# Optimization experiments

Measured on AMD Instinct MI355X. Metric: run time of the kernel, lower is better.

Reference implementation:

```python
import jax, jax.numpy as jnp
import numpy as np

D = 64
H = 4
HD = D // H
N_MOL, E_MOL = 2048, 32768
N_PROT, E_PROT = 8192, 262144
LN_EPS = 1e-5


def _lin_params(key, d_in, d_out):
    k1, k2 = jax.random.split(key)
    lim = 1.0 / np.sqrt(d_in)
    w = jax.random.uniform(k1, (d_in, d_out), minval=-lim, maxval=lim, dtype=jnp.float32)
    b = jax.random.uniform(k2, (d_out,), minval=-lim, maxval=lim, dtype=jnp.float32)
    return w, b


def setup_inputs() -> dict:
    key = jax.random.key(0)
    ks = jax.random.split(key, 20)
    inp = {
        'x_mol': jax.random.normal(ks[0], (N_MOL, D), dtype=jnp.float32),
        'edge_index_mol': jax.random.randint(ks[1], (2, E_MOL), 0, N_MOL),
        'edge_attr_mol': jax.random.normal(ks[2], (E_MOL, D), dtype=jnp.float32),
        'x_prot': jax.random.normal(ks[3], (N_PROT, D), dtype=jnp.float32),
        'edge_index_prot': jax.random.randint(ks[4], (2, E_PROT), 0, N_PROT),
        'edge_attr_prot': jax.random.normal(ks[5], (E_PROT, D), dtype=jnp.float32),
    }
    # GINE MLPs: Linear -> ReLU -> Linear
    inp['mol_w1'], inp['mol_b1'] = _lin_params(ks[6], D, D)
    inp['mol_w2'], inp['mol_b2'] = _lin_params(ks[7], D, D)
    inp['prot_w1'], inp['prot_b1'] = _lin_params(ks[8], D, D)
    inp['prot_w2'], inp['prot_b2'] = _lin_params(ks[9], D, D)
    # cross-attn mol->prot (query=mol, key/value=prot)
    inp['mp_wq'], inp['mp_bq'] = _lin_params(ks[10], D, D)
    inp['mp_wk'], inp['mp_bk'] = _lin_params(ks[11], D, D)
    inp['mp_wv'], inp['mp_bv'] = _lin_params(ks[12], D, D)
    # cross-attn prot->mol (query=prot, key/value=mol)
    inp['pm_wq'], inp['pm_bq'] = _lin_params(ks[13], D, D)
    inp['pm_wk'], inp['pm_bk'] = _lin_params(ks[14], D, D)
    inp['pm_wv'], inp['pm_bv'] = _lin_params(ks[15], D, D)
    # layer norms
    inp['ln_mol_g'] = jnp.ones((D,), jnp.float32)
    inp['ln_mol_b'] = jnp.zeros((D,), jnp.float32)
    inp['ln_prot_g'] = jnp.ones((D,), jnp.float32)
    inp['ln_prot_b'] = jnp.zeros((D,), jnp.float32)
    return inp


def _gine_conv(x, edge_index, edge_attr, w1, b1, w2, b2, n_nodes):
    # message: relu(x_j + edge_attr); aggregate: mean at target; update: MLP((1+eps)*x + aggr), eps=0
    src, dst = edge_index[0], edge_index[1]
    msg = jax.nn.relu(x[src] + edge_attr)                       # [E, D]
    ssum = jax.ops.segment_sum(msg, dst, num_segments=n_nodes)  # [N, D]
    cnt = jax.ops.segment_sum(jnp.ones((msg.shape[0],), msg.dtype), dst, num_segments=n_nodes)
    aggr = ssum / jnp.maximum(cnt, 1.0)[:, None]
    h = x + aggr
    h = jax.nn.relu(h @ w1 + b1) @ w2 + b2
    return h


def _cross_attn(q_nodes, k_nodes, wq, bq, wk, bk, wv, bv):
    Nq, Nk = q_nodes.shape[0], k_nodes.shape[0]
    Q = (q_nodes @ wq + bq).reshape(Nq, H, HD)
    K = (k_nodes @ wk + bk).reshape(Nk, H, HD)
    V = (k_nodes @ wv + bv).reshape(Nk, H, HD)
    scores = jnp.einsum('qhd,khd->hqk', Q, K) / np.sqrt(HD).astype(np.float32)
    attn = jax.nn.softmax(scores, axis=-1)                      # [H, Nq, Nk]
    out = jnp.einsum('hqk,khd->qhd', attn, V).reshape(Nq, D)
    return out


def _layer_norm(x, g, b):
    mu = jnp.mean(x, axis=-1, keepdims=True)
    var = jnp.mean(jnp.square(x - mu), axis=-1, keepdims=True)
    return (x - mu) * jax.lax.rsqrt(var + LN_EPS) * g + b


def reference(x_mol, edge_index_mol, edge_attr_mol, x_prot, edge_index_prot, edge_attr_prot,
              mol_w1, mol_b1, mol_w2, mol_b2, prot_w1, prot_b1, prot_w2, prot_b2,
              mp_wq, mp_bq, mp_wk, mp_bk, mp_wv, mp_bv,
              pm_wq, pm_bq, pm_wk, pm_bk, pm_wv, pm_bv,
              ln_mol_g, ln_mol_b, ln_prot_g, ln_prot_b):
    h_mol = jax.nn.relu(_gine_conv(x_mol, edge_index_mol, edge_attr_mol,
                                   mol_w1, mol_b1, mol_w2, mol_b2, x_mol.shape[0]))
    h_prot = jax.nn.relu(_gine_conv(x_prot, edge_index_prot, edge_attr_prot,
                                    prot_w1, prot_b1, prot_w2, prot_b2, x_prot.shape[0]))
    h_mol_attn = _cross_attn(h_mol, h_prot, mp_wq, mp_bq, mp_wk, mp_bk, mp_wv, mp_bv)
    h_prot_attn = _cross_attn(h_prot, h_mol, pm_wq, pm_bq, pm_wk, pm_bk, pm_wv, pm_bv)
    out_mol = _layer_norm(h_mol + h_mol_attn, ln_mol_g, ln_mol_b)
    out_prot = _layer_norm(h_prot + h_prot_attn, ln_prot_g, ln_prot_b)
    return out_mol, out_prot
```

## Files before the change

kernel.cpp:

```cpp
#include <hip/hip_runtime.h>

#define NM 2048
#define EM 32768
#define NP 8192
#define EP 262144

typedef __attribute__((ext_vector_type(8))) short short8;
typedef __attribute__((ext_vector_type(4))) short short4v;
typedef __attribute__((ext_vector_type(4))) float f32x4;
typedef __attribute__((ext_vector_type(16))) float f32x16;

#define LOG2E 1.44269504088896340736f

__device__ __forceinline__ float e2(float x) { return __builtin_amdgcn_exp2f(x); }
__device__ __forceinline__ unsigned int pk_bf16_tr(float a, float b) {
    return __builtin_amdgcn_perm(__float_as_uint(a), __float_as_uint(b), 0x03020706u);
}
__device__ __forceinline__ unsigned short cvt_bf16(float f) {
    unsigned int u = __float_as_uint(f);
    u = (u + 0x7fff + ((u >> 16) & 1)) >> 16;
    return (unsigned short)u;
}

__global__ __launch_bounds__(256) void hist_kernel(
    const int* __restrict__ ei_m, const int* __restrict__ ei_p,
    int* __restrict__ cnt_m, int* __restrict__ cnt_p)
{
    int idx = blockIdx.x * 256 + threadIdx.x;
    if (idx < EM) atomicAdd(&cnt_m[ei_m[EM + idx]], 1);
    int j = idx - EM;
    if (j >= 0 && j < EP) atomicAdd(&cnt_p[ei_p[EP + j]], 1);
}

__global__ __launch_bounds__(256) void scan_kernel(
    const int* __restrict__ cnt_m, const int* __restrict__ cnt_p,
    int* __restrict__ start_m, int* __restrict__ start_p,
    int* __restrict__ cur_m, int* __restrict__ cur_p)
{
    const int* cnt; int* start; int* cur; int n;
    if (blockIdx.x == 0) { cnt = cnt_m; start = start_m; cur = cur_m; n = NM; }
    else                 { cnt = cnt_p; start = start_p; cur = cur_p; n = NP; }
    int per = n >> 8;
    int tid = threadIdx.x;
    int base = tid * per;
    int s = 0;
    for (int i = 0; i < per; i++) s += cnt[base + i];
    __shared__ int wsum[4];
    int lane = tid & 63, w = tid >> 6;
    int v = s;
    #pragma unroll
    for (int off = 1; off < 64; off <<= 1) {
        int u = __shfl_up(v, off, 64);
        if (lane >= off) v += u;
    }
    if (lane == 63) wsum[w] = v;
    __syncthreads();
    int wo = 0;
    for (int i = 0; i < w; i++) wo += wsum[i];
    int run = wo + v - s;
    for (int i = 0; i < per; i++) {
        start[base + i] = run; cur[base + i] = run;
        run += cnt[base + i];
    }
    if (tid == 255) start[n] = run;
}

__global__ __launch_bounds__(256) void scatter_kernel(
    const int* __restrict__ ei_m, const int* __restrict__ ei_p,
    int* __restrict__ cur_m, int* __restrict__ cur_p,
    int* __restrict__ pidx_m, int* __restrict__ pidx_p)
{
    int idx = blockIdx.x * 256 + threadIdx.x;
    if (idx < EM) {
        int d = ei_m[EM + idx];
        int pos = atomicAdd(&cur_m[d], 1);
        pidx_m[pos] = (idx << 11) | ei_m[idx];
    }
    int j = idx - EM;
    if (j >= 0 && j < EP) {
        int d = ei_p[EP + j];
        int pos = atomicAdd(&cur_p[d], 1);
        pidx_p[pos] = (j << 13) | ei_p[j];
    }
}

__global__ __launch_bounds__(256) void node_aggr_kernel(
    const float* __restrict__ x_m, const float* __restrict__ ea_m,
    const int* __restrict__ start_m, const int* __restrict__ pidx_m,
    const float* __restrict__ x_p, const float* __restrict__ ea_p,
    const int* __restrict__ start_p, const int* __restrict__ pidx_p,
    unsigned short* __restrict__ h0b_m, unsigned short* __restrict__ h0b_p)
{
    int wave = threadIdx.x >> 6, lane = threadIdx.x & 63;
    int nid = blockIdx.x * 4 + wave;
    const float *x, *ea; const int *start, *pidx; unsigned short* h0b; int n, sh, msk;
    if (nid < NM) { x = x_m; ea = ea_m; start = start_m; pidx = pidx_m; h0b = h0b_m; n = nid; sh = 11; msk = 2047; }
    else          { x = x_p; ea = ea_p; start = start_p; pidx = pidx_p; h0b = h0b_p; n = nid - NM; sh = 13; msk = 8191; }
    int b  = __builtin_amdgcn_readfirstlane(start[n]);
    int e  = __builtin_amdgcn_readfirstlane(start[n + 1]);
    int deg = e - b;
    const int* pp = pidx + b;
    float acc = 0.f;
    int j = 0;
    for (; j + 8 <= deg; j += 8) {
        int v0 = __builtin_amdgcn_readfirstlane(pp[j]);
        int v1 = __builtin_amdgcn_readfirstlane(pp[j + 1]);
        int v2 = __builtin_amdgcn_readfirstlane(pp[j + 2]);
        int v3 = __builtin_amdgcn_readfirstlane(pp[j + 3]);
        int v4 = __builtin_amdgcn_readfirstlane(pp[j + 4]);
        int v5 = __builtin_amdgcn_readfirstlane(pp[j + 5]);
        int v6 = __builtin_amdgcn_readfirstlane(pp[j + 6]);
        int v7 = __builtin_amdgcn_readfirstlane(pp[j + 7]);
        float a0 = ea[(size_t)(((unsigned)v0) >> sh) * 64 + lane];
        float a1 = ea[(size_t)(((unsigned)v1) >> sh) * 64 + lane];
        float a2 = ea[(size_t)(((unsigned)v2) >> sh) * 64 + lane];
        float a3 = ea[(size_t)(((unsigned)v3) >> sh) * 64 + lane];
        float a4 = ea[(size_t)(((unsigned)v4) >> sh) * 64 + lane];
        float a5 = ea[(size_t)(((unsigned)v5) >> sh) * 64 + lane];
        float a6 = ea[(size_t)(((unsigned)v6) >> sh) * 64 + lane];
        float a7 = ea[(size_t)(((unsigned)v7) >> sh) * 64 + lane];
        float y0 = x[(size_t)(v0 & msk) * 64 + lane];
        float y1 = x[(size_t)(v1 & msk) * 64 + lane];
        float y2 = x[(size_t)(v2 & msk) * 64 + lane];
        float y3 = x[(size_t)(v3 & msk) * 64 + lane];
        float y4 = x[(size_t)(v4 & msk) * 64 + lane];
        float y5 = x[(size_t)(v5 & msk) * 64 + lane];
        float y6 = x[(size_t)(v6 & msk) * 64 + lane];
        float y7 = x[(size_t)(v7 & msk) * 64 + lane];
        acc += fmaxf(y0 + a0, 0.f); acc += fmaxf(y1 + a1, 0.f);
        acc += fmaxf(y2 + a2, 0.f); acc += fmaxf(y3 + a3, 0.f);
        acc += fmaxf(y4 + a4, 0.f); acc += fmaxf(y5 + a5, 0.f);
        acc += fmaxf(y6 + a6, 0.f); acc += fmaxf(y7 + a7, 0.f);
    }
    for (; j < deg; ++j) {
        int v0 = __builtin_amdgcn_readfirstlane(pp[j]);
        acc += fmaxf(x[(size_t)(v0 & msk) * 64 + lane] + ea[(size_t)(((unsigned)v0) >> sh) * 64 + lane], 0.f);
    }
    float aggr = acc / fmaxf((float)deg, 1.f);
    h0b[(size_t)n * 64 + lane] = cvt_bf16(x[(size_t)n * 64 + lane] + aggr);
}

__global__ __launch_bounds__(256) void prep_w_kernel(
    const float* __restrict__ w0, const float* __restrict__ w1, const float* __restrict__ w2,
    const float* __restrict__ w3, const float* __restrict__ w4, const float* __restrict__ w5,
    const float* __restrict__ w6, const float* __restrict__ w7, const float* __restrict__ w8,
    const float* __restrict__ w9, unsigned short* __restrict__ wt)
{
    int b = blockIdx.x;
    int t = b >> 4;
    int e = (b & 15) * 256 + threadIdx.x;
    const float* src;
    switch (t) {
        case 0: src = w0; break; case 1: src = w1; break; case 2: src = w2; break;
        case 3: src = w3; break; case 4: src = w4; break; case 5: src = w5; break;
        case 6: src = w6; break; case 7: src = w7; break; case 8: src = w8; break;
        default: src = w9; break;
    }
    int n = e >> 6, k = e & 63;
    wt[t * 4096 + e] = cvt_bf16(src[k * 64 + n]);
}

__global__ __launch_bounds__(256) void mlp_qkv_kernel(
    const unsigned short* __restrict__ h0b_m, const unsigned short* __restrict__ h0b_p,
    const unsigned short* __restrict__ wt,
    const float* __restrict__ b1m_, const float* __restrict__ b2m_,
    const float* __restrict__ bqm_, const float* __restrict__ bkm_, const float* __restrict__ bvm_,
    const float* __restrict__ b1p_, const float* __restrict__ b2p_,
    const float* __restrict__ bqp_, const float* __restrict__ bkp_, const float* __restrict__ bvp_,
    float* __restrict__ hm, float* __restrict__ hp,
    unsigned short* __restrict__ Qm, unsigned short* __restrict__ Km, unsigned short* __restrict__ Vtm,
    unsigned short* __restrict__ Qp, unsigned short* __restrict__ Kp, unsigned short* __restrict__ Vtp,
    int* __restrict__ norms)
{
    __shared__ unsigned short tile[4][2][16][72];
    int t = threadIdx.x, wave = t >> 6, lane = t & 63;
    int col = lane & 15, quad = lane >> 4;
    int blk = blockIdx.x;
    const unsigned short* h0b; const float *b1, *b2, *bq, *bk, *bv;
    float* hout; unsigned short *Q, *K, *Vt; int N, row0, wofs, nb;
    if (blk < NM / 64) {
        h0b = h0b_m; b1 = b1m_; b2 = b2m_; bq = bqm_; bk = bkm_; bv = bvm_;
        hout = hm; Q = Qm; K = Km; Vt = Vtm; N = NM;
        row0 = blk * 64 + wave * 16; wofs = 0; nb = 0;
    } else {
        h0b = h0b_p; b1 = b1p_; b2 = b2p_; bq = bqp_; bk = bkp_; bv = bvp_;
        hout = hp; Q = Qp; K = Kp; Vt = Vtp; N = NP;
        row0 = (blk - NM / 64) * 64 + wave * 16; wofs = 5 * 4096; nb = 2;
    }
    const f32x4 zero4 = {0.f, 0.f, 0.f, 0.f};
    const unsigned short* wb = wt + wofs + (size_t)col * 64 + quad * 8;

    const unsigned short* ar = h0b + (size_t)(row0 + col) * 64 + quad * 8;
    short8 aL = *(const short8*)ar;
    short8 aH = *(const short8*)(ar + 32);

    #pragma unroll
    for (int nt = 0; nt < 4; ++nt) {
        short8 bL = *(const short8*)(wb + nt * 1024);
        short8 bH = *(const short8*)(wb + nt * 1024 + 32);
        f32x4 d = __builtin_amdgcn_mfma_f32_16x16x32_bf16(aL, bL, zero4, 0, 0, 0);
        d = __builtin_amdgcn_mfma_f32_16x16x32_bf16(aH, bH, d, 0, 0, 0);
        float bias = b1[nt * 16 + col];
        #pragma unroll
        for (int r = 0; r < 4; ++r)
            tile[wave][0][quad * 4 + r][nt * 16 + col] = cvt_bf16(fmaxf(d[r] + bias, 0.f));
    }
    short8 a1L = *(const short8*)&tile[wave][0][col][quad * 8];
    short8 a1H = *(const short8*)&tile[wave][0][col][32 + quad * 8];

    #pragma unroll
    for (int nt = 0; nt < 4; ++nt) {
        short8 bL = *(const short8*)(wb + 4096 + nt * 1024);
        short8 bH = *(const short8*)(wb + 4096 + nt * 1024 + 32);
        f32x4 d = __builtin_amdgcn_mfma_f32_16x16x32_bf16(a1L, bL, zero4, 0, 0, 0);
        d = __builtin_amdgcn_mfma_f32_16x16x32_bf16(a1H, bH, d, 0, 0, 0);
        float bias = b2[nt * 16 + col];
        #pragma unroll
        for (int r = 0; r < 4; ++r) {
            float v = fmaxf(d[r] + bias, 0.f);
            hout[(size_t)(row0 + quad * 4 + r) * 64 + nt * 16 + col] = v;
            tile[wave][1][quad * 4 + r][nt * 16 + col] = cvt_bf16(v);
        }
    }
    short8 a2L = *(const short8*)&tile[wave][1][col][quad * 8];
    short8 a2H = *(const short8*)&tile[wave][1][col][32 + quad * 8];

    float q2[4] = {0.f, 0.f, 0.f, 0.f};
    #pragma unroll
    for (int nt = 0; nt < 4; ++nt) {
        short8 bL = *(const short8*)(wb + 2 * 4096 + nt * 1024);
        short8 bH = *(const short8*)(wb + 2 * 4096 + nt * 1024 + 32);
        f32x4 d = __builtin_amdgcn_mfma_f32_16x16x32_bf16(a2L, bL, zero4, 0, 0, 0);
        d = __builtin_amdgcn_mfma_f32_16x16x32_bf16(a2H, bH, d, 0, 0, 0);
        float bias = bq[nt * 16 + col];
        #pragma unroll
        for (int r = 0; r < 4; ++r) {
            float qv = (d[r] + bias) * (0.25f * LOG2E);
            Q[(size_t)(row0 + quad * 4 + r) * 64 + nt * 16 + col] = cvt_bf16(qv);
            q2[r] += qv * qv;
        }
    }
    float qmx = 0.f;
    #pragma unroll
    for (int r = 0; r < 4; ++r) {
        float s = q2[r];
        s += __shfl_xor(s, 1, 64); s += __shfl_xor(s, 2, 64);
        s += __shfl_xor(s, 4, 64); s += __shfl_xor(s, 8, 64);
        qmx = fmaxf(qmx, s);
    }

    float k2[4] = {0.f, 0.f, 0.f, 0.f};
    #pragma unroll
    for (int nt = 0; nt < 4; ++nt) {
        short8 bL = *(const short8*)(wb + 3 * 4096 + nt * 1024);
        short8 bH = *(const short8*)(wb + 3 * 4096 + nt * 1024 + 32);
        f32x4 d = __builtin_amdgcn_mfma_f32_16x16x32_bf16(a2L, bL, zero4, 0, 0, 0);
        d = __builtin_amdgcn_mfma_f32_16x16x32_bf16(a2H, bH, d, 0, 0, 0);
        float bias = bk[nt * 16 + col];
        #pragma unroll
        for (int r = 0; r < 4; ++r) {
            float kv = d[r] + bias;
            K[(size_t)(row0 + quad * 4 + r) * 64 + nt * 16 + col] = cvt_bf16(kv);
            k2[r] += kv * kv;
        }
    }
    float kmx = 0.f;
    #pragma unroll
    for (int r = 0; r < 4; ++r) {
        float s = k2[r];
        s += __shfl_xor(s, 1, 64); s += __shfl_xor(s, 2, 64);
        s += __shfl_xor(s, 4, 64); s += __shfl_xor(s, 8, 64);
        kmx = fmaxf(kmx, s);
    }

    #pragma unroll
    for (int nt = 0; nt < 4; ++nt) {
        short8 bL = *(const short8*)(wb + 4 * 4096 + nt * 1024);
        short8 bH = *(const short8*)(wb + 4 * 4096 + nt * 1024 + 32);
        f32x4 d = __builtin_amdgcn_mfma_f32_16x16x32_bf16(a2L, bL, zero4, 0, 0, 0);
        d = __builtin_amdgcn_mfma_f32_16x16x32_bf16(a2H, bH, d, 0, 0, 0);
        float bias = bv[nt * 16 + col];
        short4v vv;
        vv.x = (short)cvt_bf16(d[0] + bias);
        vv.y = (short)cvt_bf16(d[1] + bias);
        vv.z = (short)cvt_bf16(d[2] + bias);
        vv.w = (short)cvt_bf16(d[3] + bias);
        *(short4v*)(Vt + (size_t)(nt * 16 + col) * N + row0 + quad * 4) = vv;
    }

    qmx = fmaxf(qmx, __shfl_xor(qmx, 16, 64)); qmx = fmaxf(qmx, __shfl_xor(qmx, 32, 64));
    kmx = fmaxf(kmx, __shfl_xor(kmx, 16, 64)); kmx = fmaxf(kmx, __shfl_xor(kmx, 32, 64));
    if (lane == 0) {
        atomicMax(&norms[nb],     __float_as_int(sqrtf(qmx)));
        atomicMax(&norms[nb + 1], __float_as_int(sqrtf(kmx)));
    }
}

__global__ __launch_bounds__(256) void attn_kernel(
    const unsigned short* __restrict__ Qm, const unsigned short* __restrict__ Km,
    const unsigned short* __restrict__ Vtm,
    const unsigned short* __restrict__ Qp, const unsigned short* __restrict__ Kp,
    const unsigned short* __restrict__ Vtp,
    const int* __restrict__ norms, float* __restrict__ partial)
{
    __shared__ unsigned int plds[4][2][2][16][20];
    int t = threadIdx.x;
    int wave = t >> 6;
    int lane = t & 63;
    int qrow = lane & 15;
    int quad = lane >> 4;
    int q5   = lane & 31;
    int half = lane >> 5;
    int qtl  = q5 >> 4;
    int dwb  = half * 2;
    int W = blockIdx.x * 4 + wave;

    const unsigned short *Q, *K, *Vt; int Nk; float m;
    int chunk, h, qt2, Tbase, T1off;
    if (W < 2048) {
        Q = Qm; K = Kp; Vt = Vtp; Nk = NP;
        m = __int_as_float(norms[0]) * __int_as_float(norms[3]);
        chunk = W & 7; h = (W >> 3) & 3; qt2 = W >> 5;
        Tbase = W + qt2 * 32; T1off = 32;
    } else {
        int W2 = W - 2048;
        Q = Qp; K = Km; Vt = Vtm; Nk = NM;
        m = __int_as_float(norms[2]) * __int_as_float(norms[1]);
        chunk = W2 & 1; h = (W2 >> 1) & 3; qt2 = W2 >> 3;
        Tbase = 4096 + W2 + qt2 * 8; T1off = 8;
    }

    short8 qf = *(const short8*)(Q + ((size_t)(qt2 * 32 + q5)) * 64 + h * 16 + half * 8);

    const f32x16 zero16 = {0.f,0.f,0.f,0.f,0.f,0.f,0.f,0.f,0.f,0.f,0.f,0.f,0.f,0.f,0.f,0.f};
    const f32x4 zero4 = {0.f, 0.f, 0.f, 0.f};
    int kbase = chunk * 1024;
    const unsigned short* krow = K + (size_t)(kbase + q5) * 64 + h * 16 + half * 8;
    const unsigned short* vrow = Vt + ((size_t)(h * 16 + qrow)) * Nk + kbase + quad * 8;

    float l = 0.0f;
    f32x4 accA = zero4, accB = zero4;

    short8 kf_0, kf_1, vf_0, vf_1;
    kf_0 = *(const short8*)(krow);
    kf_1 = *(const short8*)(krow + 32 * 64);
    vf_0 = *(const short8*)(vrow);
    vf_1 = *(const short8*)(vrow + 32);

    short8 vf_prev;

#define QK_PHASE(IT, SLOT, BUF)                                                             \
    {                                                                                       \
        short8 kf = kf_##SLOT; short8 vf = vf_##SLOT;                                       \
        if ((IT) < 30) {                                                                    \
            int off = ((IT) + 2) * 32;                                                      \
            kf_##SLOT = *(const short8*)(krow + (size_t)off * 64);                          \
            vf_##SLOT = *(const short8*)(vrow + off);                                       \
        }                                                                                   \
        f32x16 s = __builtin_amdgcn_mfma_f32_32x32x16_bf16(kf, qf, zero16, 0, 0, 0);        \
        float p0  = e2(s[0] - m),  p1  = e2(s[1] - m),  p2  = e2(s[2] - m),  p3  = e2(s[3] - m);  \
        float p4  = e2(s[4] - m),  p5  = e2(s[5] - m),  p6  = e2(s[6] - m),  p7  = e2(s[7] - m);  \
        float p8  = e2(s[8] - m),  p9  = e2(s[9] - m),  p10 = e2(s[10] - m), p11 = e2(s[11] - m); \
        float p12 = e2(s[12] - m), p13 = e2(s[13] - m), p14 = e2(s[14] - m), p15 = e2(s[15] - m); \
        l += (((p0 + p1) + (p2 + p3)) + ((p4 + p5) + (p6 + p7)))                            \
           + (((p8 + p9) + (p10 + p11)) + ((p12 + p13) + (p14 + p15)));                     \
        uint2 w0; w0.x = pk_bf16_tr(p0, p1);   w0.y = pk_bf16_tr(p2, p3);                   \
        uint2 w1; w1.x = pk_bf16_tr(p4, p5);   w1.y = pk_bf16_tr(p6, p7);                   \
        uint2 w2; w2.x = pk_bf16_tr(p8, p9);   w2.y = pk_bf16_tr(p10, p11);                 \
        uint2 w3; w3.x = pk_bf16_tr(p12, p13); w3.y = pk_bf16_tr(p14, p15);                 \
        *(uint2*)&plds[wave][qtl][BUF][qrow][dwb]      = w0;                                \
        *(uint2*)&plds[wave][qtl][BUF][qrow][dwb + 4]  = w1;                                \
        *(uint2*)&plds[wave][qtl][BUF][qrow][dwb + 8]  = w2;                                \
        *(uint2*)&plds[wave][qtl][BUF][qrow][dwb + 12] = w3;                                \
        vf_cur = vf;                                                                        \
    }

#define STEP(IT, SLOT, BUF, PREV)                                                           \
    {                                                                                       \
        short8 pfA = *(short8*)&plds[wave][0][PREV][qrow][quad * 4];                        \
        short8 pfB = *(short8*)&plds[wave][1][PREV][qrow][quad * 4];                        \
        short8 vf_cur;                                                                      \
        QK_PHASE(IT, SLOT, BUF)                                                             \
        accA = __builtin_amdgcn_mfma_f32_16x16x32_bf16(vf_prev, pfA, accA, 0, 0, 0);        \
        accB = __builtin_amdgcn_mfma_f32_16x16x32_bf16(vf_prev, pfB, accB, 0, 0, 0);        \
        vf_prev = vf_cur;                                                                   \
    }

    {
        short8 vf_cur;
        QK_PHASE(0, 0, 0)
        vf_prev = vf_cur;
    }
    for (int p = 0; p < 15; ++p) {
        STEP(2 * p + 1, 1, 1, 0)
        STEP(2 * p + 2, 0, 0, 1)
    }
    STEP(31, 1, 1, 0)
    {
        short8 pfA = *(short8*)&plds[wave][0][1][qrow][quad * 4];
        short8 pfB = *(short8*)&plds[wave][1][1][qrow][quad * 4];
        accA = __builtin_amdgcn_mfma_f32_16x16x32_bf16(vf_prev, pfA, accA, 0, 0, 0);
        accB = __builtin_amdgcn_mfma_f32_16x16x32_bf16(vf_prev, pfB, accB, 0, 0, 0);
    }
#undef STEP
#undef QK_PHASE

    float ltot = l + __shfl_xor(l, 32, 64);

    float* pb0 = partial + (size_t)Tbase * 288;
    *(f32x4*)&pb0[qrow * 16 + quad * 4] = accA;
    float* pb1 = partial + (size_t)(Tbase + T1off) * 288;
    *(f32x4*)&pb1[qrow * 16 + quad * 4] = accB;
    if (lane < 16)       pb0[272 + q5] = ltot;
    else if (lane < 32)  pb1[272 + (q5 - 16)] = ltot;
}

__global__ __launch_bounds__(256) void merge_ln_kernel(
    const float* __restrict__ partial,
    const float* __restrict__ h_m, const float* __restrict__ h_p,
    const float* __restrict__ gm, const float* __restrict__ bm,
    const float* __restrict__ gp, const float* __restrict__ bp_,
    float* __restrict__ out)
{
    int t = threadIdx.x;
    int grow = blockIdx.x * 4 + (t >> 6);
    int c = t & 63;
    const float *pbase, *hbuf, *g, *bb; float* o; int NC, row;
    if (grow < NM) { pbase = partial;               hbuf = h_m; g = gm; bb = bm;  o = out;             NC = 8; row = grow; }
    else           { pbase = partial + 4096 * 288;  hbuf = h_p; g = gp; bb = bp_; o = out + NM * 64;   NC = 2; row = grow - NM; }
    int hi = c >> 4, d = c & 15;
    int qt = row >> 4, ql = row & 15;
    const float* base = pbase + (size_t)(qt * 4 + hi) * NC * 288;
    float L = 0.0f, A = 0.0f;
    for (int cc = 0; cc < NC; ++cc) {
        L += base[cc * 288 + 272 + ql];
        A += base[cc * 288 + ql * 16 + d];
    }
    float v = hbuf[(size_t)row * 64 + c] + A / L;
    float s = v;
    #pragma unroll
    for (int o2 = 32; o2 >= 1; o2 >>= 1) s += __shfl_xor(s, o2, 64);
    float mu = s * (1.0f / 64.0f);
    float dv = v - mu;
    float sq = dv * dv;
    #pragma unroll
    for (int o2 = 32; o2 >= 1; o2 >>= 1) sq += __shfl_xor(sq, o2, 64);
    float var = sq * (1.0f / 64.0f);
    o[(size_t)row * 64 + c] = dv * rsqrtf(var + 1e-5f) * g[c] + bb[c];
}

extern "C" void kernel_launch(void* const* d_in, const int* in_sizes, int n_in,
                              void* d_out, int out_size, void* d_ws, size_t ws_size,
                              hipStream_t stream)
{
    const float* x_mol   = (const float*)d_in[0];
    const int*   ei_mol  = (const int*)  d_in[1];
    const float* ea_mol  = (const float*)d_in[2];
    const float* x_prot  = (const float*)d_in[3];
    const int*   ei_prot = (const int*)  d_in[4];
    const float* ea_prot = (const float*)d_in[5];
    const float* mol_w1  = (const float*)d_in[6];
    const float* mol_b1  = (const float*)d_in[7];
    const float* mol_w2  = (const float*)d_in[8];
    const float* mol_b2  = (const float*)d_in[9];
    const float* prot_w1 = (const float*)d_in[10];
    const float* prot_b1 = (const float*)d_in[11];
    const float* prot_w2 = (const float*)d_in[12];
    const float* prot_b2 = (const float*)d_in[13];
    const float* mp_wq = (const float*)d_in[14]; const float* mp_bq = (const float*)d_in[15];
    const float* mp_wk = (const float*)d_in[16]; const float* mp_bk = (const float*)d_in[17];
    const float* mp_wv = (const float*)d_in[18]; const float* mp_bv = (const float*)d_in[19];
    const float* pm_wq = (const float*)d_in[20]; const float* pm_bq = (const float*)d_in[21];
    const float* pm_wk = (const float*)d_in[22]; const float* pm_bk = (const float*)d_in[23];
    const float* pm_wv = (const float*)d_in[24]; const float* pm_bv = (const float*)d_in[25];
    const float* ln_mol_g  = (const float*)d_in[26];
    const float* ln_mol_b  = (const float*)d_in[27];
    const float* ln_prot_g = (const float*)d_in[28];
    const float* ln_prot_b = (const float*)d_in[29];

    float* ws = (float*)d_ws;
    float* h_mol   = ws;
    float* h_prot  = h_mol + 131072;
    float* partial = h_prot + 524288;
    unsigned short* h0b_mol  = (unsigned short*)partial;
    unsigned short* h0b_prot = h0b_mol + 131072;
    int* ip      = (int*)(partial + 2359296);
    int* cnt_m   = ip;
    int* cnt_p   = cnt_m + 2048;
    int* norms   = cnt_p + 8192;
    int* start_m = norms + 4;
    int* start_p = start_m + 2052;
    int* cur_m   = start_p + 8196;
    int* cur_p   = cur_m + 2048;
    int* pidx_m  = cur_p + 8192;
    int* pidx_p  = pidx_m + 32768;
    unsigned short* bf = (unsigned short*)(pidx_p + 262144);
    unsigned short* Qm  = bf;
    unsigned short* Km  = Qm + 131072;
    unsigned short* Vtm = Km + 131072;
    unsigned short* Qp  = Vtm + 131072;
    unsigned short* Kp  = Qp + 524288;
    unsigned short* Vtp = Kp + 524288;
    unsigned short* wt  = Vtp + 524288;

    hipMemsetAsync(cnt_m, 0, (size_t)(2048 + 8192 + 4) * sizeof(int), stream);

    prep_w_kernel<<<160, 256, 0, stream>>>(
        mol_w1, mol_w2, mp_wq, pm_wk, pm_wv,
        prot_w1, prot_w2, pm_wq, mp_wk, mp_wv, wt);

    const int EB = (EM + EP) / 256;
    hist_kernel<<<EB, 256, 0, stream>>>(ei_mol, ei_prot, cnt_m, cnt_p);
    scan_kernel<<<2, 256, 0, stream>>>(cnt_m, cnt_p, start_m, start_p, cur_m, cur_p);
    scatter_kernel<<<EB, 256, 0, stream>>>(ei_mol, ei_prot, cur_m, cur_p, pidx_m, pidx_p);
    node_aggr_kernel<<<(NM + NP) / 4, 256, 0, stream>>>(
        x_mol, ea_mol, start_m, pidx_m,
        x_prot, ea_prot, start_p, pidx_p, h0b_mol, h0b_prot);

    mlp_qkv_kernel<<<(NM + NP) / 64, 256, 0, stream>>>(
        h0b_mol, h0b_prot, wt,
        mol_b1, mol_b2, mp_bq, pm_bk, pm_bv,
        prot_b1, prot_b2, pm_bq, mp_bk, mp_bv,
        h_mol, h_prot, Qm, Km, Vtm, Qp, Kp, Vtp, norms);

    attn_kernel<<<1024, 256, 0, stream>>>(Qm, Km, Vtm, Qp, Kp, Vtp, norms, partial);

    float* out = (float*)d_out;
    merge_ln_kernel<<<(NM + NP) / 4, 256, 0, stream>>>(
        partial, h_mol, h_prot, ln_mol_g, ln_mol_b, ln_prot_g, ln_prot_b, out);
}
```

Before: 290.3 us.

## Fuse weight prep into histogram, shrink MLP blocks, double attention key-split chunks

Merges the weight-transpose kernel into the histogram kernel to save one launch. Shrinks the MLP/QKV blocks to a single wave each, giving four times as many blocks. Halves the key chunk length in the attention kernel (512 keys instead of 1024), doubling the number of waves and partial results, with the merge/layernorm kernel adjusted to reduce over more chunks. This targets more parallelism and latency hiding, in exchange for a larger partial buffer, more merge reads and extra softmax rescale overhead.

```diff
diff --git a/kernel.cpp b/kernel.cpp
--- a/kernel.cpp
+++ b/kernel.cpp
@@ -22,11 +22,30 @@
     return (unsigned short)u;
 }
 
-__global__ __launch_bounds__(256) void hist_kernel(
+__global__ __launch_bounds__(256) void prep_hist_kernel(
+    const float* __restrict__ w0, const float* __restrict__ w1, const float* __restrict__ w2,
+    const float* __restrict__ w3, const float* __restrict__ w4, const float* __restrict__ w5,
+    const float* __restrict__ w6, const float* __restrict__ w7, const float* __restrict__ w8,
+    const float* __restrict__ w9, unsigned short* __restrict__ wt,
     const int* __restrict__ ei_m, const int* __restrict__ ei_p,
     int* __restrict__ cnt_m, int* __restrict__ cnt_p)
 {
-    int idx = blockIdx.x * 256 + threadIdx.x;
+    int b = blockIdx.x;
+    if (b < 160) {
+        int t = b >> 4;
+        int e = (b & 15) * 256 + threadIdx.x;
+        const float* src;
+        switch (t) {
+            case 0: src = w0; break; case 1: src = w1; break; case 2: src = w2; break;
+            case 3: src = w3; break; case 4: src = w4; break; case 5: src = w5; break;
+            case 6: src = w6; break; case 7: src = w7; break; case 8: src = w8; break;
+            default: src = w9; break;
+        }
+        int n = e >> 6, k = e & 63;
+        wt[t * 4096 + e] = cvt_bf16(src[k * 64 + n]);
+        return;
+    }
+    int idx = (b - 160) * 256 + threadIdx.x;
     if (idx < EM) atomicAdd(&cnt_m[ei_m[EM + idx]], 1);
     int j = idx - EM;
     if (j >= 0 && j < EP) atomicAdd(&cnt_p[ei_p[EP + j]], 1);
@@ -140,27 +159,7 @@
     h0b[(size_t)n * 64 + lane] = cvt_bf16(x[(size_t)n * 64 + lane] + aggr);
 }
 
-__global__ __launch_bounds__(256) void prep_w_kernel(
-    const float* __restrict__ w0, const float* __restrict__ w1, const float* __restrict__ w2,
-    const float* __restrict__ w3, const float* __restrict__ w4, const float* __restrict__ w5,
-    const float* __restrict__ w6, const float* __restrict__ w7, const float* __restrict__ w8,
-    const float* __restrict__ w9, unsigned short* __restrict__ wt)
-{
-    int b = blockIdx.x;
-    int t = b >> 4;
-    int e = (b & 15) * 256 + threadIdx.x;
-    const float* src;
-    switch (t) {
-        case 0: src = w0; break; case 1: src = w1; break; case 2: src = w2; break;
-        case 3: src = w3; break; case 4: src = w4; break; case 5: src = w5; break;
-        case 6: src = w6; break; case 7: src = w7; break; case 8: src = w8; break;
-        default: src = w9; break;
-    }
-    int n = e >> 6, k = e & 63;
-    wt[t * 4096 + e] = cvt_bf16(src[k * 64 + n]);
-}
-
-__global__ __launch_bounds__(256) void mlp_qkv_kernel(
+__global__ __launch_bounds__(64) void mlp_qkv_kernel(
     const unsigned short* __restrict__ h0b_m, const unsigned short* __restrict__ h0b_p,
     const unsigned short* __restrict__ wt,
     const float* __restrict__ b1m_, const float* __restrict__ b2m_,
@@ -172,20 +171,20 @@
     unsigned short* __restrict__ Qp, unsigned short* __restrict__ Kp, unsigned short* __restrict__ Vtp,
     int* __restrict__ norms)
 {
-    __shared__ unsigned short tile[4][2][16][72];
-    int t = threadIdx.x, wave = t >> 6, lane = t & 63;
+    __shared__ unsigned short tile[2][16][72];
+    int lane = threadIdx.x & 63;
     int col = lane & 15, quad = lane >> 4;
     int blk = blockIdx.x;
     const unsigned short* h0b; const float *b1, *b2, *bq, *bk, *bv;
     float* hout; unsigned short *Q, *K, *Vt; int N, row0, wofs, nb;
-    if (blk < NM / 64) {
+    if (blk < NM / 16) {
         h0b = h0b_m; b1 = b1m_; b2 = b2m_; bq = bqm_; bk = bkm_; bv = bvm_;
         hout = hm; Q = Qm; K = Km; Vt = Vtm; N = NM;
-        row0 = blk * 64 + wave * 16; wofs = 0; nb = 0;
+        row0 = blk * 16; wofs = 0; nb = 0;
     } else {
         h0b = h0b_p; b1 = b1p_; b2 = b2p_; bq = bqp_; bk = bkp_; bv = bvp_;
         hout = hp; Q = Qp; K = Kp; Vt = Vtp; N = NP;
-        row0 = (blk - NM / 64) * 64 + wave * 16; wofs = 5 * 4096; nb = 2;
+        row0 = (blk - NM / 16) * 16; wofs = 5 * 4096; nb = 2;
     }
     const f32x4 zero4 = {0.f, 0.f, 0.f, 0.f};
     const unsigned short* wb = wt + wofs + (size_t)col * 64 + quad * 8;
@@ -203,10 +202,10 @@
         float bias = b1[nt * 16 + col];
         #pragma unroll
         for (int r = 0; r < 4; ++r)
-            tile[wave][0][quad * 4 + r][nt * 16 + col] = cvt_bf16(fmaxf(d[r] + bias, 0.f));
-    }
-    short8 a1L = *(const short8*)&tile[wave][0][col][quad * 8];
-    short8 a1H = *(const short8*)&tile[wave][0][col][32 + quad * 8];
+            tile[0][quad * 4 + r][nt * 16 + col] = cvt_bf16(fmaxf(d[r] + bias, 0.f));
+    }
+    short8 a1L = *(const short8*)&tile[0][col][quad * 8];
+    short8 a1H = *(const short8*)&tile[0][col][32 + quad * 8];
 
     #pragma unroll
     for (int nt = 0; nt < 4; ++nt) {
@@ -219,11 +218,11 @@
         for (int r = 0; r < 4; ++r) {
             float v = fmaxf(d[r] + bias, 0.f);
             hout[(size_t)(row0 + quad * 4 + r) * 64 + nt * 16 + col] = v;
-            tile[wave][1][quad * 4 + r][nt * 16 + col] = cvt_bf16(v);
+            tile[1][quad * 4 + r][nt * 16 + col] = cvt_bf16(v);
         }
     }
-    short8 a2L = *(const short8*)&tile[wave][1][col][quad * 8];
-    short8 a2H = *(const short8*)&tile[wave][1][col][32 + quad * 8];
+    short8 a2L = *(const short8*)&tile[1][col][quad * 8];
+    short8 a2H = *(const short8*)&tile[1][col][32 + quad * 8];
 
     float q2[4] = {0.f, 0.f, 0.f, 0.f};
     #pragma unroll
@@ -317,24 +316,24 @@
 
     const unsigned short *Q, *K, *Vt; int Nk; float m;
     int chunk, h, qt2, Tbase, T1off;
-    if (W < 2048) {
+    if (W < 4096) {
         Q = Qm; K = Kp; Vt = Vtp; Nk = NP;
         m = __int_as_float(norms[0]) * __int_as_float(norms[3]);
-        chunk = W & 7; h = (W >> 3) & 3; qt2 = W >> 5;
-        Tbase = W + qt2 * 32; T1off = 32;
+        chunk = W & 15; h = (W >> 4) & 3; qt2 = W >> 6;
+        Tbase = W + qt2 * 64; T1off = 64;
     } else {
-        int W2 = W - 2048;
+        int W2 = W - 4096;
         Q = Qp; K = Km; Vt = Vtm; Nk = NM;
         m = __int_as_float(norms[2]) * __int_as_float(norms[1]);
-        chunk = W2 & 1; h = (W2 >> 1) & 3; qt2 = W2 >> 3;
-        Tbase = 4096 + W2 + qt2 * 8; T1off = 8;
+        chunk = W2 & 3; h = (W2 >> 2) & 3; qt2 = W2 >> 4;
+        Tbase = 8192 + W2 + qt2 * 16; T1off = 16;
     }
 
     short8 qf = *(const short8*)(Q + ((size_t)(qt2 * 32 + q5)) * 64 + h * 16 + half * 8);
 
     const f32x16 zero16 = {0.f,0.f,0.f,0.f,0.f,0.f,0.f,0.f,0.f,0.f,0.f,0.f,0.f,0.f,0.f,0.f};
     const f32x4 zero4 = {0.f, 0.f, 0.f, 0.f};
-    int kbase = chunk * 1024;
+    int kbase = chunk * 512;
     const unsigned short* krow = K + (size_t)(kbase + q5) * 64 + h * 16 + half * 8;
     const unsigned short* vrow = Vt + ((size_t)(h * 16 + qrow)) * Nk + kbase + quad * 8;
 
@@ -352,7 +351,7 @@
 #define QK_PHASE(IT, SLOT, BUF)                                                             \
     {                                                                                       \
         short8 kf = kf_##SLOT; short8 vf = vf_##SLOT;                                       \
-        if ((IT) < 30) {                                                                    \
+        if ((IT) < 14) {                                                                    \
             int off = ((IT) + 2) * 32;                                                      \
             kf_##SLOT = *(const short8*)(krow + (size_t)off * 64);                          \
             vf_##SLOT = *(const short8*)(vrow + off);                                       \
@@ -391,11 +390,11 @@
         QK_PHASE(0, 0, 0)
         vf_prev = vf_cur;
     }
-    for (int p = 0; p < 15; ++p) {
+    for (int p = 0; p < 7; ++p) {
         STEP(2 * p + 1, 1, 1, 0)
         STEP(2 * p + 2, 0, 0, 1)
     }
-    STEP(31, 1, 1, 0)
+    STEP(15, 1, 1, 0)
     {
         short8 pfA = *(short8*)&plds[wave][0][1][qrow][quad * 4];
         short8 pfB = *(short8*)&plds[wave][1][1][qrow][quad * 4];
@@ -426,8 +425,8 @@
     int grow = blockIdx.x * 4 + (t >> 6);
     int c = t & 63;
     const float *pbase, *hbuf, *g, *bb; float* o; int NC, row;
-    if (grow < NM) { pbase = partial;               hbuf = h_m; g = gm; bb = bm;  o = out;             NC = 8; row = grow; }
-    else           { pbase = partial + 4096 * 288;  hbuf = h_p; g = gp; bb = bp_; o = out + NM * 64;   NC = 2; row = grow - NM; }
+    if (grow < NM) { pbase = partial;               hbuf = h_m; g = gm; bb = bm;  o = out;            NC = 16; row = grow; }
+    else           { pbase = partial + 8192 * 288;  hbuf = h_p; g = gp; bb = bp_; o = out + NM * 64;  NC = 4;  row = grow - NM; }
     int hi = c >> 4, d = c & 15;
     int qt = row >> 4, ql = row & 15;
     const float* base = pbase + (size_t)(qt * 4 + hi) * NC * 288;
@@ -484,7 +483,7 @@
     float* partial = h_prot + 524288;
     unsigned short* h0b_mol  = (unsigned short*)partial;
     unsigned short* h0b_prot = h0b_mol + 131072;
-    int* ip      = (int*)(partial + 2359296);
+    int* ip      = (int*)(partial + 4718592);
     int* cnt_m   = ip;
     int* cnt_p   = cnt_m + 2048;
     int* norms   = cnt_p + 8192;
@@ -505,25 +504,24 @@
 
     hipMemsetAsync(cnt_m, 0, (size_t)(2048 + 8192 + 4) * sizeof(int), stream);
 
-    prep_w_kernel<<<160, 256, 0, stream>>>(
+    const int EB = (EM + EP) / 256;
+    prep_hist_kernel<<<160 + EB, 256, 0, stream>>>(
         mol_w1, mol_w2, mp_wq, pm_wk, pm_wv,
-        prot_w1, prot_w2, pm_wq, mp_wk, mp_wv, wt);
-
-    const int EB = (EM + EP) / 256;
-    hist_kernel<<<EB, 256, 0, stream>>>(ei_mol, ei_prot, cnt_m, cnt_p);
+        prot_w1, prot_w2, pm_wq, mp_wk, mp_wv, wt,
+        ei_mol, ei_prot, cnt_m, cnt_p);
     scan_kernel<<<2, 256, 0, stream>>>(cnt_m, cnt_p, start_m, start_p, cur_m, cur_p);
     scatter_kernel<<<EB, 256, 0, stream>>>(ei_mol, ei_prot, cur_m, cur_p, pidx_m, pidx_p);
     node_aggr_kernel<<<(NM + NP) / 4, 256, 0, stream>>>(
         x_mol, ea_mol, start_m, pidx_m,
         x_prot, ea_prot, start_p, pidx_p, h0b_mol, h0b_prot);
 
-    mlp_qkv_kernel<<<(NM + NP) / 64, 256, 0, stream>>>(
+    mlp_qkv_kernel<<<(NM + NP) / 16, 64, 0, stream>>>(
         h0b_mol, h0b_prot, wt,
         mol_b1, mol_b2, mp_bq, pm_bk, pm_bv,
         prot_b1, prot_b2, pm_bq, mp_bk, mp_bv,
         h_mol, h_prot, Qm, Km, Vtm, Qp, Kp, Vtp, norms);
 
-    attn_kernel<<<1024, 256, 0, stream>>>(Qm, Km, Vtm, Qp, Kp, Vtp, norms, partial);
+    attn_kernel<<<2048, 256, 0, stream>>>(Qm, Km, Vtm, Qp, Kp, Vtp, norms, partial);
 
     float* out = (float*)d_out;
     merge_ln_kernel<<<(NM + NP) / 4, 256, 0, stream>>>(
```

After: 292.9 us. About the same (+0.9%).
